# Kernel optimization log

Hardware: AMD Instinct MI355X
Metric: run time of the kernel (lower is better)

## Reference

```python
import jax, jax.numpy as jnp
import numpy as np

D_MODEL = 512
NUM_HEADS = 8
D_K = D_MODEL // NUM_HEADS
LN_EPS = 1e-5


def setup_inputs() -> dict:
    key = jax.random.key(0)
    ks = jax.random.split(key, 11)
    d = D_MODEL
    s = 1.0 / np.sqrt(d)
    return {
        "x": jax.random.normal(ks[0], (4, 2048, d), dtype=jnp.float32),
        "Wq": jax.random.uniform(ks[1], (d, d), jnp.float32, -s, s),
        "bq": jax.random.uniform(ks[2], (d,), jnp.float32, -s, s),
        "Wk": jax.random.uniform(ks[3], (d, d), jnp.float32, -s, s),
        "bk": jax.random.uniform(ks[4], (d,), jnp.float32, -s, s),
        "Wv": jax.random.uniform(ks[5], (d, d), jnp.float32, -s, s),
        "bv": jax.random.uniform(ks[6], (d,), jnp.float32, -s, s),
        "Wo": jax.random.uniform(ks[7], (d, d), jnp.float32, -s, s),
        "bo": jax.random.uniform(ks[8], (d,), jnp.float32, -s, s),
        "gamma": jnp.ones((d,), jnp.float32),
        "beta": jnp.zeros((d,), jnp.float32),
    }


def reference(x, Wq, bq, Wk, bk, Wv, bv, Wo, bo, gamma, beta):
    # x: (B, S, D). Dropout is identity (eval mode).
    B, S, D = x.shape
    H, dk = NUM_HEADS, D_K
    # Linear layers use torch convention: y = x @ W.T + b
    q = (x @ Wq.T + bq).reshape(B, S, H, dk).transpose(0, 2, 1, 3)  # (B,H,S,dk)
    k = (x @ Wk.T + bk).reshape(B, S, H, dk).transpose(0, 2, 1, 3)
    v = (x @ Wv.T + bv).reshape(B, S, H, dk).transpose(0, 2, 1, 3)
    scores = jnp.einsum("bhqd,bhkd->bhqk", q, k) / jnp.sqrt(jnp.float32(dk))
    attn = jax.nn.softmax(scores, axis=-1)
    ctx = jnp.einsum("bhqk,bhkd->bhqd", attn, v)  # (B,H,S,dk)
    ctx = ctx.transpose(0, 2, 1, 3).reshape(B, S, D)
    out = ctx @ Wo.T + bo
    # residual + LayerNorm
    y = x + out
    mu = jnp.mean(y, axis=-1, keepdims=True)
    var = jnp.mean(jnp.square(y - mu), axis=-1, keepdims=True)
    return (y - mu) / jnp.sqrt(var + LN_EPS) * gamma + beta
```

## Files before the change

kernel.cpp:

```cpp
#include <hip/hip_runtime.h>
#include <math.h>

#define D 512
#define NH 8
#define DK 64
#define S 2048
#define BATCH 4
#define N_TOK (BATCH * S)

#define QSCALE 0.18033688f

typedef __bf16 bf16x8 __attribute__((ext_vector_type(8)));
typedef __bf16 bf16x4 __attribute__((ext_vector_type(4)));
typedef float f32x4 __attribute__((ext_vector_type(4)));

#define AS1 __attribute__((address_space(1)))
#define AS3 __attribute__((address_space(3)))

#define OFF_XB   0
#define OFF_WB   8388608
#define OFF_Q    10485760
#define OFF_K    18874368
#define OFF_VT   27262976
#define OFF_CTX  35651584
#define OFF_Y    10485760
#define OFF_FLAG 44040192

static __device__ __forceinline__ bf16x8 ldg8(const __bf16* p) {
    return *(const bf16x8*)p;
}
static __device__ __forceinline__ f32x4 mfma16(bf16x8 a, bf16x8 b, f32x4 c) {
    return __builtin_amdgcn_mfma_f32_16x16x32_bf16(a, b, c, 0, 0, 0);
}
static __device__ __forceinline__ float ldf(const void* p, size_t i, int isf) {
    return isf ? ((const float*)p)[i] : (float)(((const __bf16*)p)[i]);
}
static __device__ __forceinline__ float fexp2(float x) {
#if __has_builtin(__builtin_amdgcn_exp2f)
    return __builtin_amdgcn_exp2f(x);
#else
    return exp2f(x);
#endif
}
static __device__ __forceinline__ unsigned pack_trunc(float e0, float e1) {
    return (__builtin_bit_cast(unsigned, e0) >> 16)
         | (__builtin_bit_cast(unsigned, e1) & 0xFFFF0000u);
}
static __device__ __forceinline__ void gload_lds16(const void* g, void* l) {
    __builtin_amdgcn_global_load_lds((const AS1 char*)g, (AS3 char*)l, 16, 0, 0);
}

__global__ __launch_bounds__(256)
void cvt_kernel(const void* __restrict__ x,  const void* __restrict__ Wq,
                const void* __restrict__ Wk, const void* __restrict__ Wv,
                const void* __restrict__ Wo, __bf16* __restrict__ xb,
                __bf16* __restrict__ Wb, int* __restrict__ flag)
{
    const bf16x8 probe = ldg8((const __bf16*)x + (threadIdx.x & 63) * 8);
    int bad = 0;
#pragma unroll
    for (int j = 0; j < 8; ++j) bad |= !(fabsf((float)probe[j]) <= 64.0f);
    const int isf = __any(bad) ? 1 : 0;
    if (blockIdx.x == 0 && threadIdx.x == 0) *flag = isf;

    const size_t i0 = ((size_t)blockIdx.x * 256 + threadIdx.x) * 8;
    const void* src;
    __bf16* dst;
    size_t off;
    if (i0 < 4194304) {
        src = x; off = i0; dst = xb + i0;
    } else {
        const size_t wrel = i0 - 4194304;
        const size_t w = wrel >> 18;
        src = (w == 0) ? Wq : (w == 1) ? Wk : (w == 2) ? Wv : Wo;
        off = wrel & 262143;
        dst = Wb + wrel;
    }
    bf16x8 r;
    if (isf) {
        const float* f = (const float*)src + off;
#pragma unroll
        for (int j = 0; j < 8; ++j) r[j] = (__bf16)f[j];
    } else {
        r = *(const bf16x8*)((const __bf16*)src + off);
    }
    *(bf16x8*)dst = r;
}

__global__ __launch_bounds__(256)
void qkv_kernel(const __bf16* __restrict__ xb, const __bf16* __restrict__ Wb,
                const void* __restrict__ bq, const void* __restrict__ bk,
                const void* __restrict__ bv, const int* __restrict__ flag,
                __bf16* __restrict__ Q, __bf16* __restrict__ K,
                __bf16* __restrict__ Vt)
{
    __shared__ __align__(16) char smem[32768];

    const int isf = *flag;
    const int tid = threadIdx.x;
    const int w = tid >> 6, l = tid & 63;
    const int lane16 = l & 15, quad = l >> 4;
    const int wm = w >> 1, wn = w & 1;
    const int m0 = blockIdx.x * 128;
    const int by = blockIdx.y;
    const int n0 = by * 128;

    const int cwl = w * 64 + l;
    const int g0 = (cwl & 3) ^ ((cwl >> 3) & 3);
    const __bf16* aS0 = xb + (size_t)(m0 + (cwl >> 2)) * D + g0 * 8;
    const __bf16* aS1 = aS0 + (size_t)64 * D;
    const __bf16* bS0 = Wb + (size_t)(n0 + (cwl >> 2)) * D + g0 * 8;
    const __bf16* bS1 = bS0 + (size_t)64 * D;

    const int sw = (quad ^ ((lane16 >> 1) & 3)) * 16;
    const int aoff = (wm * 64 + lane16) * 64 + sw;
    const int boff = 8192 + (wn * 64 + lane16) * 64 + sw;

    f32x4 acc[4][4];
#pragma unroll
    for (int i = 0; i < 4; ++i)
#pragma unroll
        for (int j = 0; j < 4; ++j) acc[i][j] = (f32x4){0,0,0,0};

    gload_lds16(aS0, smem + w * 1024);
    gload_lds16(aS1, smem + 4096 + w * 1024);
    gload_lds16(bS0, smem + 8192 + w * 1024);
    gload_lds16(bS1, smem + 12288 + w * 1024);

    for (int kt = 0; kt < D / 32; ++kt) {
        __syncthreads();

        const char* bufp = smem + (kt & 1) * 16384;
        if (kt + 1 < D / 32) {
            char* nb = smem + ((kt + 1) & 1) * 16384;
            gload_lds16(aS0 + (kt + 1) * 32, nb + w * 1024);
            gload_lds16(aS1 + (kt + 1) * 32, nb + 4096 + w * 1024);
            gload_lds16(bS0 + (kt + 1) * 32, nb + 8192 + w * 1024);
            gload_lds16(bS1 + (kt + 1) * 32, nb + 12288 + w * 1024);
        }

        bf16x8 af[4], bf[4];
#pragma unroll
        for (int i = 0; i < 4; ++i) af[i] = *(const bf16x8*)(bufp + aoff + i * 1024);
#pragma unroll
        for (int j = 0; j < 4; ++j) bf[j] = *(const bf16x8*)(bufp + boff + j * 1024);
#pragma unroll
        for (int i = 0; i < 4; ++i)
#pragma unroll
            for (int j = 0; j < 4; ++j)
                acc[i][j] = mfma16(af[i], bf[j], acc[i][j]);
    }

    const int which = by >> 2;
    const int h = (by * 2 + wn) & 7;
    const float qs = (which == 0) ? QSCALE : 1.0f;
    const void* bias = (which == 0) ? bq : (which == 1) ? bk : bv;
    float bvv[4];
#pragma unroll
    for (int j = 0; j < 4; ++j)
        bvv[j] = ldf(bias, ((by & 3) * 128 + wn * 64 + 16 * j + lane16) & 511, isf);

    const int bb = m0 >> 11;
    const int ssb = (m0 & (S - 1)) + wm * 64;

    if (which < 2) {
        __bf16* out = ((which == 0) ? Q : K) + ((size_t)(bb * NH + h) * S) * DK;
#pragma unroll
        for (int i = 0; i < 4; ++i)
#pragma unroll
            for (int r = 0; r < 4; ++r) {
                const int ss = ssb + i * 16 + quad * 4 + r;
#pragma unroll
                for (int j = 0; j < 4; ++j)
                    out[(size_t)ss * DK + 16 * j + lane16] =
                        (__bf16)((acc[i][j][r] + bvv[j]) * qs);
            }
    } else {
#pragma unroll
        for (int i = 0; i < 4; ++i)
#pragma unroll
            for (int j = 0; j < 4; ++j) {
                const int dkc = 16 * j + lane16;
                __bf16* vp = Vt + ((size_t)(bb * NH + h) * DK + dkc) * S
                                + ssb + i * 16 + quad * 4;
                bf16x4 pkt;
#pragma unroll
                for (int r = 0; r < 4; ++r) pkt[r] = (__bf16)(acc[i][j][r] + bvv[j]);
                *(bf16x4*)vp = pkt;
            }
    }
}

__global__ __launch_bounds__(256)
void attn_kernel(const __bf16* __restrict__ Q, const __bf16* __restrict__ K,
                 const __bf16* __restrict__ Vt, __bf16* __restrict__ ctx)
{
    __shared__ __align__(16) char smem[49152];

    const int tid = threadIdx.x;
    const int w = tid >> 6, l = tid & 63;
    const int lane16 = l & 15, quad = l >> 4;

    const int lin = blockIdx.x;
    const int xcd = lin & 7;
    const int t = lin >> 3;
    const int bh = xcd * 4 + (t >> 4);
    const int qt = t & 15;
    const int b = bh >> 3, h = bh & 7;
    const size_t bhS = (size_t)bh * S;

    const int cwl = w * 64 + l;
    const char* kS[2];
    const char* vS[2];
#pragma unroll
    for (int c = 0; c < 2; ++c) {
        const int s = c * 256 + cwl;
        const int row = s >> 3;
        const int g = (s & 7) ^ (row & 7);
        kS[c] = (const char*)(K + (bhS + row) * DK) + g * 16;
        vS[c] = (const char*)(Vt + ((size_t)bh * DK + row) * S) + g * 16;
    }

    const int qbase = qt * 128 + w * 32;
    bf16x8 qa[2][2];
#pragma unroll
    for (int u = 0; u < 2; ++u) {
        const __bf16* Qp = Q + (bhS + qbase + u * 16 + lane16) * DK + quad * 8;
        qa[u][0] = ldg8(Qp);
        qa[u][1] = ldg8(Qp + 32);
    }

    bf16x8 aones;
#pragma unroll
    for (int j = 0; j < 8; ++j) aones[j] = (__bf16)1.0f;

    const int x7 = lane16 & 7;
    char* pw = smem + 32768 + w * 4096;
    const int pwoff = lane16 * 128 + ((quad & 1) * 8);
    const int proff = lane16 * 128;

    f32x4 o[2][4], lacc[2];
#pragma unroll
    for (int u = 0; u < 2; ++u) {
        lacc[u] = (f32x4){0,0,0,0};
#pragma unroll
        for (int tt = 0; tt < 4; ++tt) o[u][tt] = (f32x4){0,0,0,0};
    }

    gload_lds16(kS[0], smem + w * 1024);
    gload_lds16(kS[1], smem + 4096 + w * 1024);
    gload_lds16(vS[0], smem + 8192 + w * 1024);
    gload_lds16(vS[1], smem + 12288 + w * 1024);

    for (int kc = 0; kc < S / 64; ++kc) {
        __syncthreads();

        const int buf = kc & 1;
        const char* kb = smem + buf * 16384;
        const char* vb = kb + 8192;

        if (kc + 1 < S / 64) {
            char* kb2 = smem + (buf ^ 1) * 16384;
            gload_lds16(kS[0] + (size_t)(kc + 1) * 8192, kb2 + w * 1024);
            gload_lds16(kS[1] + (size_t)(kc + 1) * 8192, kb2 + 4096 + w * 1024);
            gload_lds16(vS[0] + (size_t)(kc + 1) * 128, kb2 + 8192 + w * 1024);
            gload_lds16(vS[1] + (size_t)(kc + 1) * 128, kb2 + 12288 + w * 1024);
        }

        bf16x8 kfA[4], kfB[4];
#pragma unroll
        for (int tt = 0; tt < 4; ++tt) {
            const int base = (tt * 16 + lane16) * 128;
            kfA[tt] = *(const bf16x8*)(kb + base + ((quad ^ x7) * 16));
            kfB[tt] = *(const bf16x8*)(kb + base + (((quad + 4) ^ x7) * 16));
        }

#pragma unroll
        for (int u = 0; u < 2; ++u) {
            f32x4 st[4];
#pragma unroll
            for (int tt = 0; tt < 4; ++tt) {
                f32x4 z = {0,0,0,0};
                z = mfma16(kfA[tt], qa[u][0], z);
                st[tt] = mfma16(kfB[tt], qa[u][1], z);
            }
#pragma unroll
            for (int tt = 0; tt < 4; ++tt) {
                uint2 pkt;
                pkt.x = pack_trunc(fexp2(st[tt][0]), fexp2(st[tt][1]));
                pkt.y = pack_trunc(fexp2(st[tt][2]), fexp2(st[tt][3]));
                *(uint2*)(pw + u * 2048 + pwoff
                          + (((tt * 2 + (quad >> 1)) ^ x7) * 16)) = pkt;
            }
        }

        bf16x8 vA[4], vB[4];
#pragma unroll
        for (int tt = 0; tt < 4; ++tt) {
            const int base = (tt * 16 + lane16) * 128;
            vA[tt] = *(const bf16x8*)(vb + base + ((quad ^ x7) * 16));
            vB[tt] = *(const bf16x8*)(vb + base + (((quad + 4) ^ x7) * 16));
        }
#pragma unroll
        for (int u = 0; u < 2; ++u) {
            const bf16x8 bp0 = *(const bf16x8*)(pw + u * 2048 + proff
                                                + (((0 + quad) ^ x7) * 16));
            const bf16x8 bp1 = *(const bf16x8*)(pw + u * 2048 + proff
                                                + (((4 + quad) ^ x7) * 16));
            lacc[u] = mfma16(aones, bp0, lacc[u]);
            lacc[u] = mfma16(aones, bp1, lacc[u]);
#pragma unroll
            for (int tt = 0; tt < 4; ++tt) {
                o[u][tt] = mfma16(vA[tt], bp0, o[u][tt]);
                o[u][tt] = mfma16(vB[tt], bp1, o[u][tt]);
            }
        }
    }

#pragma unroll
    for (int u = 0; u < 2; ++u) {
        const float inv = 1.0f / lacc[u][0];
        __bf16* cp = ctx + ((size_t)(b * S + qbase + u * 16 + lane16)) * D
                     + h * DK;
#pragma unroll
        for (int tt = 0; tt < 4; ++tt) {
            bf16x4 pkt;
#pragma unroll
            for (int r = 0; r < 4; ++r) pkt[r] = (__bf16)(o[u][tt][r] * inv);
            *(bf16x4*)(cp + tt * 16 + quad * 4) = pkt;
        }
    }
}

__global__ __launch_bounds__(256)
void proj_kernel(const __bf16* __restrict__ ctx, const __bf16* __restrict__ Wb,
                 const void* __restrict__ bo, const __bf16* __restrict__ xb,
                 const int* __restrict__ flag, __bf16* __restrict__ y)
{
    __shared__ __align__(16) char smem[24576];

    const int isf = *flag;
    const int tid = threadIdx.x;
    const int w = tid >> 6, l = tid & 63;
    const int lane16 = l & 15, quad = l >> 4;
    const int wm = w >> 1, wn = w & 1;
    const int m0 = blockIdx.x * 64;
    const int n0 = blockIdx.y * 128;

    const __bf16* Wo = Wb + (size_t)3 * 262144;
    const int cwl = w * 64 + l;
    const int g0 = (cwl & 3) ^ ((cwl >> 3) & 3);
    const __bf16* aS = ctx + (size_t)(m0 + (cwl >> 2)) * D + g0 * 8;
    const __bf16* bS0 = Wo + (size_t)(n0 + (cwl >> 2)) * D + g0 * 8;
    const __bf16* bS1 = bS0 + (size_t)64 * D;

    const int sw = (quad ^ ((lane16 >> 1) & 3)) * 16;
    const int aoff = (wm * 32 + lane16) * 64 + sw;
    const int boff = 4096 + (wn * 64 + lane16) * 64 + sw;

    f32x4 acc[2][4];
#pragma unroll
    for (int i = 0; i < 2; ++i)
#pragma unroll
        for (int j = 0; j < 4; ++j) acc[i][j] = (f32x4){0,0,0,0};

    gload_lds16(aS, smem + w * 1024);
    gload_lds16(bS0, smem + 4096 + w * 1024);
    gload_lds16(bS1, smem + 8192 + w * 1024);

    for (int kt = 0; kt < D / 32; ++kt) {
        __syncthreads();

        const char* bufp = smem + (kt & 1) * 12288;
        if (kt + 1 < D / 32) {
            char* nb = smem + ((kt + 1) & 1) * 12288;
            gload_lds16(aS + (kt + 1) * 32, nb + w * 1024);
            gload_lds16(bS0 + (kt + 1) * 32, nb + 4096 + w * 1024);
            gload_lds16(bS1 + (kt + 1) * 32, nb + 8192 + w * 1024);
        }

        bf16x8 af[2], bf[4];
#pragma unroll
        for (int i = 0; i < 2; ++i) af[i] = *(const bf16x8*)(bufp + aoff + i * 1024);
#pragma unroll
        for (int j = 0; j < 4; ++j) bf[j] = *(const bf16x8*)(bufp + boff + j * 1024);
#pragma unroll
        for (int i = 0; i < 2; ++i)
#pragma unroll
            for (int j = 0; j < 4; ++j)
                acc[i][j] = mfma16(af[i], bf[j], acc[i][j]);
    }

    float bvv[4];
#pragma unroll
    for (int j = 0; j < 4; ++j)
        bvv[j] = ldf(bo, n0 + wn * 64 + 16 * j + lane16, isf);

#pragma unroll
    for (int i = 0; i < 2; ++i)
#pragma unroll
        for (int r = 0; r < 4; ++r) {
            const int tok = m0 + wm * 32 + i * 16 + quad * 4 + r;
#pragma unroll
            for (int j = 0; j < 4; ++j) {
                const size_t idx = (size_t)tok * D + n0 + wn * 64 + 16 * j + lane16;
                y[idx] = (__bf16)(acc[i][j][r] + bvv[j] + (float)xb[idx]);
            }
        }
}

__global__ __launch_bounds__(256)
void ln_kernel(const __bf16* __restrict__ y, const void* __restrict__ gamma,
               const void* __restrict__ beta, const int* __restrict__ flag,
               void* __restrict__ out)
{
    const int isf = *flag;
    const int l = threadIdx.x & 63;
    const int tok = blockIdx.x * 4 + (threadIdx.x >> 6);
    const bf16x8 vv = ldg8(y + (size_t)tok * D + l * 8);

    float v[8];
    float sum = 0.f, sq = 0.f;
#pragma unroll
    for (int j = 0; j < 8; ++j) {
        v[j] = (float)vv[j];
        sum += v[j];
        sq  += v[j] * v[j];
    }
#pragma unroll
    for (int msk = 1; msk < 64; msk <<= 1) {
        sum += __shfl_xor(sum, msk);
        sq  += __shfl_xor(sq,  msk);
    }
    const float mean = sum * (1.0f / D);
    const float var  = sq * (1.0f / D) - mean * mean;
    const float rstd = rsqrtf(var + 1e-5f);

    const size_t base = (size_t)tok * D + l * 8;
#pragma unroll
    for (int j = 0; j < 8; ++j) {
        const float g  = ldf(gamma, l * 8 + j, isf);
        const float be = ldf(beta,  l * 8 + j, isf);
        const float r  = ((v[j] - mean) * rstd) * g + be;
        if (isf) ((float*)out)[base + j] = r;
        else     ((__bf16*)out)[base + j] = (__bf16)r;
    }
}

extern "C" void kernel_launch(void* const* d_in, const int* in_sizes, int n_in,
                              void* d_out, int out_size, void* d_ws,
                              size_t ws_size, hipStream_t stream)
{
    const void* x     = d_in[0];
    const void* Wq    = d_in[1];
    const void* bq    = d_in[2];
    const void* Wk    = d_in[3];
    const void* bk    = d_in[4];
    const void* Wv    = d_in[5];
    const void* bv    = d_in[6];
    const void* Wo    = d_in[7];
    const void* bo    = d_in[8];
    const void* gamma = d_in[9];
    const void* beta  = d_in[10];

    char* ws = (char*)d_ws;
    __bf16* xb  = (__bf16*)(ws + OFF_XB);
    __bf16* Wb  = (__bf16*)(ws + OFF_WB);
    __bf16* Qb  = (__bf16*)(ws + OFF_Q);
    __bf16* Kb  = (__bf16*)(ws + OFF_K);
    __bf16* Vtb = (__bf16*)(ws + OFF_VT);
    __bf16* ctx = (__bf16*)(ws + OFF_CTX);
    __bf16* y   = (__bf16*)(ws + OFF_Y);
    int*    flag = (int*)(ws + OFF_FLAG);

    cvt_kernel<<<5242880 / (256 * 8), 256, 0, stream>>>(
        x, Wq, Wk, Wv, Wo, xb, Wb, flag);
    qkv_kernel<<<dim3(N_TOK / 128, 12), 256, 0, stream>>>(
        xb, Wb, bq, bk, bv, flag, Qb, Kb, Vtb);
    attn_kernel<<<dim3(512), 256, 0, stream>>>(Qb, Kb, Vtb, ctx);
    proj_kernel<<<dim3(N_TOK / 64, 4), 256, 0, stream>>>(
        ctx, Wb, bo, xb, flag, y);
    ln_kernel<<<dim3(N_TOK / 4), 256, 0, stream>>>(y, gamma, beta, flag, d_out);
}
```

Baseline: 191.0 us.

## Halve tile sizes in QKV, attention and projection kernels to double grid size

```diff
diff --git a/kernel.cpp b/kernel.cpp
--- a/kernel.cpp
+++ b/kernel.cpp
@@ -94,7 +94,7 @@
                 __bf16* __restrict__ Q, __bf16* __restrict__ K,
                 __bf16* __restrict__ Vt)
 {
-    __shared__ __align__(16) char smem[32768];
+    __shared__ __align__(16) char smem[24576];
 
     const int isf = *flag;
     const int tid = threadIdx.x;
@@ -103,62 +103,58 @@
     const int wm = w >> 1, wn = w & 1;
     const int m0 = blockIdx.x * 128;
     const int by = blockIdx.y;
-    const int n0 = by * 128;
 
     const int cwl = w * 64 + l;
     const int g0 = (cwl & 3) ^ ((cwl >> 3) & 3);
     const __bf16* aS0 = xb + (size_t)(m0 + (cwl >> 2)) * D + g0 * 8;
     const __bf16* aS1 = aS0 + (size_t)64 * D;
-    const __bf16* bS0 = Wb + (size_t)(n0 + (cwl >> 2)) * D + g0 * 8;
-    const __bf16* bS1 = bS0 + (size_t)64 * D;
+    const __bf16* bS  = Wb + (size_t)(by * 64 + (cwl >> 2)) * D + g0 * 8;
 
     const int sw = (quad ^ ((lane16 >> 1) & 3)) * 16;
     const int aoff = (wm * 64 + lane16) * 64 + sw;
-    const int boff = 8192 + (wn * 64 + lane16) * 64 + sw;
-
-    f32x4 acc[4][4];
+    const int boff = 8192 + (wn * 32 + lane16) * 64 + sw;
+
+    f32x4 acc[4][2];
 #pragma unroll
     for (int i = 0; i < 4; ++i)
 #pragma unroll
-        for (int j = 0; j < 4; ++j) acc[i][j] = (f32x4){0,0,0,0};
+        for (int j = 0; j < 2; ++j) acc[i][j] = (f32x4){0,0,0,0};
 
     gload_lds16(aS0, smem + w * 1024);
     gload_lds16(aS1, smem + 4096 + w * 1024);
-    gload_lds16(bS0, smem + 8192 + w * 1024);
-    gload_lds16(bS1, smem + 12288 + w * 1024);
+    gload_lds16(bS,  smem + 8192 + w * 1024);
 
     for (int kt = 0; kt < D / 32; ++kt) {
         __syncthreads();
 
-        const char* bufp = smem + (kt & 1) * 16384;
+        const char* bufp = smem + (kt & 1) * 12288;
         if (kt + 1 < D / 32) {
-            char* nb = smem + ((kt + 1) & 1) * 16384;
+            char* nb = smem + ((kt + 1) & 1) * 12288;
             gload_lds16(aS0 + (kt + 1) * 32, nb + w * 1024);
             gload_lds16(aS1 + (kt + 1) * 32, nb + 4096 + w * 1024);
-            gload_lds16(bS0 + (kt + 1) * 32, nb + 8192 + w * 1024);
-            gload_lds16(bS1 + (kt + 1) * 32, nb + 12288 + w * 1024);
-        }
-
-        bf16x8 af[4], bf[4];
+            gload_lds16(bS  + (kt + 1) * 32, nb + 8192 + w * 1024);
+        }
+
+        bf16x8 af[4], bf[2];
 #pragma unroll
         for (int i = 0; i < 4; ++i) af[i] = *(const bf16x8*)(bufp + aoff + i * 1024);
 #pragma unroll
-        for (int j = 0; j < 4; ++j) bf[j] = *(const bf16x8*)(bufp + boff + j * 1024);
+        for (int j = 0; j < 2; ++j) bf[j] = *(const bf16x8*)(bufp + boff + j * 1024);
 #pragma unroll
         for (int i = 0; i < 4; ++i)
 #pragma unroll
-            for (int j = 0; j < 4; ++j)
+            for (int j = 0; j < 2; ++j)
                 acc[i][j] = mfma16(af[i], bf[j], acc[i][j]);
     }
 
-    const int which = by >> 2;
-    const int h = (by * 2 + wn) & 7;
+    const int which = by >> 3;
+    const int h = by & 7;
     const float qs = (which == 0) ? QSCALE : 1.0f;
     const void* bias = (which == 0) ? bq : (which == 1) ? bk : bv;
-    float bvv[4];
-#pragma unroll
-    for (int j = 0; j < 4; ++j)
-        bvv[j] = ldf(bias, ((by & 3) * 128 + wn * 64 + 16 * j + lane16) & 511, isf);
+    float bvv[2];
+#pragma unroll
+    for (int j = 0; j < 2; ++j)
+        bvv[j] = ldf(bias, h * 64 + wn * 32 + 16 * j + lane16, isf);
 
     const int bb = m0 >> 11;
     const int ssb = (m0 & (S - 1)) + wm * 64;
@@ -171,16 +167,16 @@
             for (int r = 0; r < 4; ++r) {
                 const int ss = ssb + i * 16 + quad * 4 + r;
 #pragma unroll
-                for (int j = 0; j < 4; ++j)
-                    out[(size_t)ss * DK + 16 * j + lane16] =
+                for (int j = 0; j < 2; ++j)
+                    out[(size_t)ss * DK + wn * 32 + 16 * j + lane16] =
                         (__bf16)((acc[i][j][r] + bvv[j]) * qs);
             }
     } else {
 #pragma unroll
         for (int i = 0; i < 4; ++i)
 #pragma unroll
-            for (int j = 0; j < 4; ++j) {
-                const int dkc = 16 * j + lane16;
+            for (int j = 0; j < 2; ++j) {
+                const int dkc = wn * 32 + 16 * j + lane16;
                 __bf16* vp = Vt + ((size_t)(bb * NH + h) * DK + dkc) * S
                                 + ssb + i * 16 + quad * 4;
                 bf16x4 pkt;
@@ -195,7 +191,7 @@
 void attn_kernel(const __bf16* __restrict__ Q, const __bf16* __restrict__ K,
                  const __bf16* __restrict__ Vt, __bf16* __restrict__ ctx)
 {
-    __shared__ __align__(16) char smem[49152];
+    __shared__ __align__(16) char smem[40960];
 
     const int tid = threadIdx.x;
     const int w = tid >> 6, l = tid & 63;
@@ -204,8 +200,8 @@
     const int lin = blockIdx.x;
     const int xcd = lin & 7;
     const int t = lin >> 3;
-    const int bh = xcd * 4 + (t >> 4);
-    const int qt = t & 15;
+    const int bh = xcd * 4 + (t >> 5);
+    const int qt = t & 31;
     const int b = bh >> 3, h = bh & 7;
     const size_t bhS = (size_t)bh * S;
 
@@ -221,31 +217,23 @@
         vS[c] = (const char*)(Vt + ((size_t)bh * DK + row) * S) + g * 16;
     }
 
-    const int qbase = qt * 128 + w * 32;
-    bf16x8 qa[2][2];
-#pragma unroll
-    for (int u = 0; u < 2; ++u) {
-        const __bf16* Qp = Q + (bhS + qbase + u * 16 + lane16) * DK + quad * 8;
-        qa[u][0] = ldg8(Qp);
-        qa[u][1] = ldg8(Qp + 32);
-    }
+    const int qbase = qt * 64 + w * 16;
+    const __bf16* Qp = Q + (bhS + qbase + lane16) * DK + quad * 8;
+    const bf16x8 qa0 = ldg8(Qp);
+    const bf16x8 qa1 = ldg8(Qp + 32);
 
     bf16x8 aones;
 #pragma unroll
     for (int j = 0; j < 8; ++j) aones[j] = (__bf16)1.0f;
 
     const int x7 = lane16 & 7;
-    char* pw = smem + 32768 + w * 4096;
+    char* pw = smem + 32768 + w * 2048;
     const int pwoff = lane16 * 128 + ((quad & 1) * 8);
     const int proff = lane16 * 128;
 
-    f32x4 o[2][4], lacc[2];
-#pragma unroll
-    for (int u = 0; u < 2; ++u) {
-        lacc[u] = (f32x4){0,0,0,0};
-#pragma unroll
-        for (int tt = 0; tt < 4; ++tt) o[u][tt] = (f32x4){0,0,0,0};
-    }
+    f32x4 o[4], lacc = (f32x4){0,0,0,0};
+#pragma unroll
+    for (int tt = 0; tt < 4; ++tt) o[tt] = (f32x4){0,0,0,0};
 
     gload_lds16(kS[0], smem + w * 1024);
     gload_lds16(kS[1], smem + 4096 + w * 1024);
@@ -267,68 +255,42 @@
             gload_lds16(vS[1] + (size_t)(kc + 1) * 128, kb2 + 12288 + w * 1024);
         }
 
-        bf16x8 kfA[4], kfB[4];
 #pragma unroll
         for (int tt = 0; tt < 4; ++tt) {
             const int base = (tt * 16 + lane16) * 128;
-            kfA[tt] = *(const bf16x8*)(kb + base + ((quad ^ x7) * 16));
-            kfB[tt] = *(const bf16x8*)(kb + base + (((quad + 4) ^ x7) * 16));
-        }
-
-#pragma unroll
-        for (int u = 0; u < 2; ++u) {
-            f32x4 st[4];
-#pragma unroll
-            for (int tt = 0; tt < 4; ++tt) {
-                f32x4 z = {0,0,0,0};
-                z = mfma16(kfA[tt], qa[u][0], z);
-                st[tt] = mfma16(kfB[tt], qa[u][1], z);
-            }
-#pragma unroll
-            for (int tt = 0; tt < 4; ++tt) {
-                uint2 pkt;
-                pkt.x = pack_trunc(fexp2(st[tt][0]), fexp2(st[tt][1]));
-                pkt.y = pack_trunc(fexp2(st[tt][2]), fexp2(st[tt][3]));
-                *(uint2*)(pw + u * 2048 + pwoff
-                          + (((tt * 2 + (quad >> 1)) ^ x7) * 16)) = pkt;
-            }
-        }
-
-        bf16x8 vA[4], vB[4];
+            const bf16x8 kfA = *(const bf16x8*)(kb + base + ((quad ^ x7) * 16));
+            const bf16x8 kfB = *(const bf16x8*)(kb + base + (((quad + 4) ^ x7) * 16));
+            f32x4 z = {0,0,0,0};
+            z = mfma16(kfA, qa0, z);
+            const f32x4 st = mfma16(kfB, qa1, z);
+            uint2 pkt;
+            pkt.x = pack_trunc(fexp2(st[0]), fexp2(st[1]));
+            pkt.y = pack_trunc(fexp2(st[2]), fexp2(st[3]));
+            *(uint2*)(pw + pwoff + (((tt * 2 + (quad >> 1)) ^ x7) * 16)) = pkt;
+        }
+
+        const bf16x8 bp0 = *(const bf16x8*)(pw + proff + (((0 + quad) ^ x7) * 16));
+        const bf16x8 bp1 = *(const bf16x8*)(pw + proff + (((4 + quad) ^ x7) * 16));
+        lacc = mfma16(aones, bp0, lacc);
+        lacc = mfma16(aones, bp1, lacc);
 #pragma unroll
         for (int tt = 0; tt < 4; ++tt) {
             const int base = (tt * 16 + lane16) * 128;
-            vA[tt] = *(const bf16x8*)(vb + base + ((quad ^ x7) * 16));
-            vB[tt] = *(const bf16x8*)(vb + base + (((quad + 4) ^ x7) * 16));
-        }
-#pragma unroll
-        for (int u = 0; u < 2; ++u) {
-            const bf16x8 bp0 = *(const bf16x8*)(pw + u * 2048 + proff
-                                                + (((0 + quad) ^ x7) * 16));
-            const bf16x8 bp1 = *(const bf16x8*)(pw + u * 2048 + proff
-                                                + (((4 + quad) ^ x7) * 16));
-            lacc[u] = mfma16(aones, bp0, lacc[u]);
-            lacc[u] = mfma16(aones, bp1, lacc[u]);
-#pragma unroll
-            for (int tt = 0; tt < 4; ++tt) {
-                o[u][tt] = mfma16(vA[tt], bp0, o[u][tt]);
-                o[u][tt] = mfma16(vB[tt], bp1, o[u][tt]);
-            }
-        }
-    }
-
-#pragma unroll
-    for (int u = 0; u < 2; ++u) {
-        const float inv = 1.0f / lacc[u][0];
-        __bf16* cp = ctx + ((size_t)(b * S + qbase + u * 16 + lane16)) * D
-                     + h * DK;
-#pragma unroll
-        for (int tt = 0; tt < 4; ++tt) {
-            bf16x4 pkt;
-#pragma unroll
-            for (int r = 0; r < 4; ++r) pkt[r] = (__bf16)(o[u][tt][r] * inv);
-            *(bf16x4*)(cp + tt * 16 + quad * 4) = pkt;
-        }
+            const bf16x8 vA = *(const bf16x8*)(vb + base + ((quad ^ x7) * 16));
+            const bf16x8 vB = *(const bf16x8*)(vb + base + (((quad + 4) ^ x7) * 16));
+            o[tt] = mfma16(vA, bp0, o[tt]);
+            o[tt] = mfma16(vB, bp1, o[tt]);
+        }
+    }
+
+    const float inv = 1.0f / lacc[0];
+    __bf16* cp = ctx + ((size_t)(b * S + qbase + lane16)) * D + h * DK;
+#pragma unroll
+    for (int tt = 0; tt < 4; ++tt) {
+        bf16x4 pkt;
+#pragma unroll
+        for (int r = 0; r < 4; ++r) pkt[r] = (__bf16)(o[tt][r] * inv);
+        *(bf16x4*)(cp + tt * 16 + quad * 4) = pkt;
     }
 }
 
@@ -337,7 +299,7 @@
                  const void* __restrict__ bo, const __bf16* __restrict__ xb,
                  const int* __restrict__ flag, __bf16* __restrict__ y)
 {
-    __shared__ __align__(16) char smem[24576];
+    __shared__ __align__(16) char smem[16384];
 
     const int isf = *flag;
     const int tid = threadIdx.x;
@@ -345,56 +307,53 @@
     const int lane16 = l & 15, quad = l >> 4;
     const int wm = w >> 1, wn = w & 1;
     const int m0 = blockIdx.x * 64;
-    const int n0 = blockIdx.y * 128;
+    const int n0 = blockIdx.y * 64;
 
     const __bf16* Wo = Wb + (size_t)3 * 262144;
     const int cwl = w * 64 + l;
     const int g0 = (cwl & 3) ^ ((cwl >> 3) & 3);
     const __bf16* aS = ctx + (size_t)(m0 + (cwl >> 2)) * D + g0 * 8;
-    const __bf16* bS0 = Wo + (size_t)(n0 + (cwl >> 2)) * D + g0 * 8;
-    const __bf16* bS1 = bS0 + (size_t)64 * D;
+    const __bf16* bS = Wo + (size_t)(n0 + (cwl >> 2)) * D + g0 * 8;
 
     const int sw = (quad ^ ((lane16 >> 1) & 3)) * 16;
     const int aoff = (wm * 32 + lane16) * 64 + sw;
-    const int boff = 4096 + (wn * 64 + lane16) * 64 + sw;
-
-    f32x4 acc[2][4];
+    const int boff = 4096 + (wn * 32 + lane16) * 64 + sw;
+
+    f32x4 acc[2][2];
 #pragma unroll
     for (int i = 0; i < 2; ++i)
 #pragma unroll
-        for (int j = 0; j < 4; ++j) acc[i][j] = (f32x4){0,0,0,0};
+        for (int j = 0; j < 2; ++j) acc[i][j] = (f32x4){0,0,0,0};
 
     gload_lds16(aS, smem + w * 1024);
-    gload_lds16(bS0, smem + 4096 + w * 1024);
-    gload_lds16(bS1, smem + 8192 + w * 1024);
+    gload_lds16(bS, smem + 4096 + w * 1024);
 
     for (int kt = 0; kt < D / 32; ++kt) {
         __syncthreads();
 
-        const char* bufp = smem + (kt & 1) * 12288;
+        const char* bufp = smem + (kt & 1) * 8192;
         if (kt + 1 < D / 32) {
-            char* nb = smem + ((kt + 1) & 1) * 12288;
+            char* nb = smem + ((kt + 1) & 1) * 8192;
             gload_lds16(aS + (kt + 1) * 32, nb + w * 1024);
-            gload_lds16(bS0 + (kt + 1) * 32, nb + 4096 + w * 1024);
-            gload_lds16(bS1 + (kt + 1) * 32, nb + 8192 + w * 1024);
-        }
-
-        bf16x8 af[2], bf[4];
+            gload_lds16(bS + (kt + 1) * 32, nb + 4096 + w * 1024);
+        }
+
+        bf16x8 af[2], bf[2];
 #pragma unroll
         for (int i = 0; i < 2; ++i) af[i] = *(const bf16x8*)(bufp + aoff + i * 1024);
 #pragma unroll
-        for (int j = 0; j < 4; ++j) bf[j] = *(const bf16x8*)(bufp + boff + j * 1024);
+        for (int j = 0; j < 2; ++j) bf[j] = *(const bf16x8*)(bufp + boff + j * 1024);
 #pragma unroll
         for (int i = 0; i < 2; ++i)
 #pragma unroll
-            for (int j = 0; j < 4; ++j)
+            for (int j = 0; j < 2; ++j)
                 acc[i][j] = mfma16(af[i], bf[j], acc[i][j]);
     }
 
-    float bvv[4];
-#pragma unroll
-    for (int j = 0; j < 4; ++j)
-        bvv[j] = ldf(bo, n0 + wn * 64 + 16 * j + lane16, isf);
+    float bvv[2];
+#pragma unroll
+    for (int j = 0; j < 2; ++j)
+        bvv[j] = ldf(bo, n0 + wn * 32 + 16 * j + lane16, isf);
 
 #pragma unroll
     for (int i = 0; i < 2; ++i)
@@ -402,8 +361,8 @@
         for (int r = 0; r < 4; ++r) {
             const int tok = m0 + wm * 32 + i * 16 + quad * 4 + r;
 #pragma unroll
-            for (int j = 0; j < 4; ++j) {
-                const size_t idx = (size_t)tok * D + n0 + wn * 64 + 16 * j + lane16;
+            for (int j = 0; j < 2; ++j) {
+                const size_t idx = (size_t)tok * D + n0 + wn * 32 + 16 * j + lane16;
                 y[idx] = (__bf16)(acc[i][j][r] + bvv[j] + (float)xb[idx]);
             }
         }
@@ -475,10 +434,10 @@
 
     cvt_kernel<<<5242880 / (256 * 8), 256, 0, stream>>>(
         x, Wq, Wk, Wv, Wo, xb, Wb, flag);
-    qkv_kernel<<<dim3(N_TOK / 128, 12), 256, 0, stream>>>(
+    qkv_kernel<<<dim3(N_TOK / 128, 24), 256, 0, stream>>>(
         xb, Wb, bq, bk, bv, flag, Qb, Kb, Vtb);
-    attn_kernel<<<dim3(512), 256, 0, stream>>>(Qb, Kb, Vtb, ctx);
-    proj_kernel<<<dim3(N_TOK / 64, 4), 256, 0, stream>>>(
+    attn_kernel<<<dim3(1024), 256, 0, stream>>>(Qb, Kb, Vtb, ctx);
+    proj_kernel<<<dim3(N_TOK / 64, D / 64), 256, 0, stream>>>(
         ctx, Wb, bo, xb, flag, y);
     ln_kernel<<<dim3(N_TOK / 4), 256, 0, stream>>>(y, gamma, beta, flag, d_out);
 }
```

After: 192.4 us. No clear change (+0.7%).
